# Optimization experiments

Hardware: AMD Instinct MI355X
Metric: run time of the kernel (lower is better)

## Reference

```python
import jax, jax.numpy as jnp
from jax import lax
import numpy as np

B, H, W, C = 4, 64, 64, 128
L = H * W
DI = 2 * C   # mamba d_inner (expand=2)
NS = 16      # d_state
R = C // 16  # dt_rank
K = 4        # d_conv
S = 4        # scan branches: fwd, bwd, extra1, extra2


def setup_inputs():
    key = jax.random.key(0)
    ks = jax.random.split(key, 20)
    g = lambda i, shape, s=0.02: jax.random.normal(ks[i], shape, jnp.float32) * s
    return {
        "I1": jax.random.normal(ks[0], (B, L, C), jnp.float32),
        "fusion_resi": jax.random.normal(ks[1], (B, L, C), jnp.float32),
        "I2": jax.random.normal(ks[2], (B, L, C), jnp.float32),
        "fusion": jax.random.normal(ks[3], (B, L, C), jnp.float32),
        "ln1_w": jnp.ones((C,)), "ln1_b": jnp.zeros((C,)),
        "ln2_w": jnp.ones((C,)), "ln2_b": jnp.zeros((C,)),
        "ln3_w": jnp.ones((C,)), "ln3_b": jnp.zeros((C,)),
        "sp_w": g(4, (1, 2, 5, 5), 0.1),
        "ca_w1": g(5, (C // 4, C), 0.05),
        "ca_w2": g(6, (C, C // 4), 0.05),
        "dw_w": g(7, (C, 1, 3, 3), 0.1),
        "dw_b": jnp.zeros((C,)),
        "in_proj_w": g(8, (2 * DI, C)),
        "in_proj1_w": g(9, (DI, C)),
        "in_proj2_w": g(10, (DI, C)),
        "conv_w": g(11, (S, DI, K), 0.1),
        "conv_b": jnp.zeros((S, DI)),
        "xproj_w": g(12, (S, R + 2 * NS, DI)),
        "dt_w": g(13, (S, DI, R), 0.1),
        "dt_b": jnp.full((S, DI), -4.6, jnp.float32),  # softplus -> dt ~ 0.01
        "A_log": jnp.broadcast_to(jnp.log(jnp.arange(1, NS + 1, dtype=jnp.float32)), (S, DI, NS)) * 1.0,
        "Dskip": jnp.ones((S, DI)),
        "out_w": g(14, (C, DI)),
        "test_h": H, "test_w": W,
    }


def ln(x, w, b):
    mu = x.mean(-1, keepdims=True)
    xc = x - mu
    v = (xc * xc).mean(-1, keepdims=True)
    return xc / jnp.sqrt(v + 1e-5) * w + b


def sp_att(x, w, h, wd):
    # x: (B, N, C) -> (B, N, 1) spatial attention map
    Bb = x.shape[0]
    m = jnp.concatenate([x.mean(2, keepdims=True), x.max(2, keepdims=True)], 2)
    m = m.transpose(0, 2, 1).reshape(Bb, 2, h, wd)
    o = lax.conv_general_dilated(m, w, (1, 1), [(2, 2), (2, 2)],
                                 dimension_numbers=("NCHW", "OIHW", "NCHW"))
    return jax.nn.sigmoid(o).reshape(Bb, 1, -1).transpose(0, 2, 1)


def mamba_m3(xf, e1, e2, in_proj_w, in_proj1_w, in_proj2_w, conv_w, conv_b,
             xproj_w, dt_w, dt_b, A_log, Dskip, out_w):
    Bb, Ll, _ = xf.shape
    xz = xf @ in_proj_w.T                       # (B,L,2DI)
    x, z = xz[..., :DI], xz[..., DI:]
    # 4 branches: forward, backward (flipped), extra_emb1, extra_emb2
    u = jnp.stack([x, x[:, ::-1], e1 @ in_proj1_w.T, e2 @ in_proj2_w.T], 0)  # (S,B,L,DI)

    def causal_dwconv(xb, w, b):                # xb (B,L,DI)
        xp = jnp.pad(xb.transpose(0, 2, 1), ((0, 0), (0, 0), (K - 1, 0)))
        o = lax.conv_general_dilated(xp, w[:, None, :], (1,), "VALID",
                                     feature_group_count=DI,
                                     dimension_numbers=("NCH", "OIH", "NCH"))
        return (o + b[None, :, None]).transpose(0, 2, 1)

    uc = jax.nn.silu(jax.vmap(causal_dwconv)(u, conv_w, conv_b))        # (S,B,L,DI)
    proj = jnp.einsum("sbld,spd->sblp", uc, xproj_w)
    dt = jax.nn.softplus(jnp.einsum("sblr,sdr->sbld", proj[..., :R], dt_w)
                         + dt_b[:, None, None, :])                      # (S,B,L,DI)
    Bm, Cm = proj[..., R:R + NS], proj[..., R + NS:]                    # (S,B,L,NS)
    A = -jnp.exp(A_log)                                                 # (S,DI,NS)

    def step(h, inp):
        dt_t, B_t, C_t, u_t = inp                                       # (S,B,DI),(S,B,NS),(S,B,NS),(S,B,DI)
        dA = jnp.exp(dt_t[..., None] * A[:, None])                      # (S,B,DI,NS)
        h = h * dA + (dt_t * u_t)[..., None] * B_t[:, :, None, :]
        return h, jnp.einsum("sbdn,sbn->sbd", h, C_t)

    xs = tuple(t.transpose(2, 0, 1, 3) for t in (dt, Bm, Cm, uc))
    h0 = jnp.zeros((S, Bb, DI, NS), xf.dtype)
    _, ys = lax.scan(step, h0, xs)                                      # (L,S,B,DI)
    y = ys.transpose(1, 2, 0, 3) + uc * Dskip[:, None, None, :]         # (S,B,L,DI)
    y_tot = y[0] + y[1][:, ::-1] + y[2] + y[3]
    return (y_tot * jax.nn.silu(z)) @ out_w.T


def reference(I1, fusion_resi, I2, fusion, ln1_w, ln1_b, ln2_w, ln2_b, ln3_w,
              ln3_b, sp_w, ca_w1, ca_w2, dw_w, dw_b, in_proj_w, in_proj1_w,
              in_proj2_w, conv_w, conv_b, xproj_w, dt_w, dt_b, A_log, Dskip,
              out_w, test_h, test_w):
    fusion_resi = fusion + fusion_resi
    fusion = ln(fusion_resi, ln1_w, ln1_b)
    I2 = ln(I2 * sp_att(I2, sp_w, test_h, test_w), ln2_w, ln2_b)
    I1 = ln(I1 * sp_att(I1, sp_w, test_h, test_w), ln3_w, ln3_b)
    # note: original applies norm1/norm2/norm3 a second time here (faithful)
    gf = mamba_m3(ln(fusion, ln1_w, ln1_b), ln(I2, ln2_w, ln2_b),
                  ln(I1, ln3_w, ln3_b), in_proj_w, in_proj1_w, in_proj2_w,
                  conv_w, conv_b, xproj_w, dt_w, dt_b, A_log, Dskip, out_w)
    Bb, _, Cc = gf.shape
    f4 = gf.transpose(0, 2, 1).reshape(Bb, Cc, test_h, test_w)
    # ChannelAttention1 (already returns x*sig) then extra *fusion per source
    fc = lambda v: jnp.maximum(v @ ca_w1.T, 0.0) @ ca_w2.T
    sig = jax.nn.sigmoid(fc(f4.mean((2, 3))) + fc(f4.max((2, 3))))[:, :, None, None]
    f4 = (f4 * sig) * f4
    dw = lax.conv_general_dilated(f4, dw_w, (1, 1), [(1, 1), (1, 1)],
                                  feature_group_count=Cc,
                                  dimension_numbers=("NCHW", "OIHW", "NCHW"))
    dw = dw + dw_b[None, :, None, None]
    out = (dw + f4).reshape(Bb, Cc, -1).transpose(0, 2, 1)
    return out, fusion_resi
```

## Files before the change

kernel.cpp:

```cpp
#include <hip/hip_runtime.h>

#define DEVI __device__ __forceinline__

static constexpr int BB=4, CC=128, LLn=4096, DI=256, NS=16, RR=8, SS=4;
static constexpr int PP = RR + 2*NS;
static constexpr int CT = 64, NCH = LLn/CT;
static constexpr size_t BLC  = (size_t)BB*LLn*CC;
static constexpr size_t BLD  = (size_t)BB*LLn*DI;
static constexpr size_t SBLD = (size_t)SS*BLD;
static constexpr size_t SBLP = (size_t)SS*BB*LLn*PP;

static constexpr int OW_LN1W=0, OW_LN1B=128, OW_LN2W=256, OW_LN2B=384, OW_LN3W=512, OW_LN3B=640,
 OW_SPW=768, OW_CAW1=820, OW_CAW2=4916, OW_DWW=9012, OW_DWB=10164, OW_IPW=10292,
 OW_IP1W=75828, OW_IP2W=108596, OW_CVW=141364, OW_CVB=145460, OW_XPW=146484,
 OW_DTW=187444, OW_DTB=195636, OW_ALOG=196660, OW_DSK=213044, OW_OUTW=214068;
static constexpr int NW_RAW = 246836;
static constexpr int NW_END = 246848;

__constant__ int c_woff[22] = {OW_LN1W,OW_LN1B,OW_LN2W,OW_LN2B,OW_LN3W,OW_LN3B,OW_SPW,OW_CAW1,
 OW_CAW2,OW_DWW,OW_DWB,OW_IPW,OW_IP1W,OW_IP2W,OW_CVW,OW_CVB,OW_XPW,OW_DTW,OW_DTB,OW_ALOG,
 OW_DSK,OW_OUTW};
__constant__ int c_wsz[22]  = {128,128,128,128,128,128,50,4096,4096,1152,128,65536,32768,32768,
 4096,1024,40960,8192,1024,16384,1024,32768};

static constexpr size_t O_XF   = NW_END;
static constexpr size_t O_E1   = O_XF + BLC;
static constexpr size_t O_E2   = O_E1 + BLC;
static constexpr size_t O_Z    = O_E2 + BLC;
static constexpr size_t O_U    = O_Z + BLD;
static constexpr size_t O_UC   = O_U + SBLD;
static constexpr size_t O_PROJ = O_UC + SBLD;
static constexpr size_t O_SDT  = O_PROJ + SBLP;
static constexpr size_t O_H    = O_SDT + (size_t)SS*BB*NCH*DI;
static constexpr size_t O_M    = O_H + (size_t)SS*BB*NCH*DI*NS;
static constexpr size_t O_S    = O_M + 2*(size_t)BB*2*LLn;
static constexpr size_t O_GF   = O_S + 2*(size_t)BB*LLn;
static constexpr size_t O_PART = O_GF + BLC;
static constexpr size_t O_SIG  = O_PART + 2*(size_t)BB*32*CC;
static constexpr size_t WS_END = O_SIG + (size_t)BB*CC;

typedef __attribute__((ext_vector_type(8))) short short8v;
typedef __attribute__((ext_vector_type(4))) float f32x4;

DEVI float bfu2f(unsigned short s){ union{unsigned u; float f;} c; c.u = ((unsigned)s)<<16; return c.f; }
DEVI unsigned short f2bfu(float f){ union{float f; unsigned u;} c; c.f=f;
  unsigned r = c.u + 0x7FFFu + ((c.u>>16)&1u); return (unsigned short)(r>>16); }
DEVI bool bfmode(const void* ln1w){ return *(const unsigned*)ln1w == 0x3F803F80u; }
DEVI float2 ldin2(const void* p, int i, bool isbf){
  if(isbf){ unsigned v = *(const unsigned*)((const unsigned short*)p + i);
    return make_float2(bfu2f((unsigned short)(v & 0xFFFFu)), bfu2f((unsigned short)(v >> 16))); }
  const float* f = (const float*)p + i; return make_float2(f[0], f[1]);
}
DEVI float wsum(float v){
#pragma unroll
  for(int o=32;o;o>>=1) v += __shfl_xor(v,o,64);
  return v; }
DEVI float wmaxr(float v){
#pragma unroll
  for(int o=32;o;o>>=1) v = fmaxf(v, __shfl_xor(v,o,64));
  return v; }
DEVI float sigf(float x){ return 1.f/(1.f+__expf(-x)); }
DEVI float2 ln_wave(float2 x, const float* Wf, int ow, int ob, int lane){
  float mu = wsum(x.x + x.y) * (1.f/(float)CC);
  float dx = x.x - mu, dy = x.y - mu;
  float var = wsum(dx*dx + dy*dy) * (1.f/(float)CC);
  float rs = rsqrtf(var + 1e-5f);
  int c = 2*lane;
  return make_float2(dx*rs*Wf[ow+c] + Wf[ob+c], dy*rs*Wf[ow+c+1] + Wf[ob+c+1]);
}

struct Srcs { const void* p[22]; };

__global__ void k_xwpad(unsigned* __restrict__ xw32){
  int i = blockIdx.x*256 + threadIdx.x;
  xw32[i] = 0u;
}

__global__ void k_wcvt(Srcs s, float* __restrict__ ws,
                       unsigned short* __restrict__ wip, unsigned short* __restrict__ wob,
                       unsigned short* __restrict__ xw){
  bool isbf = bfmode(s.p[0]);
  int idx = blockIdx.x*256 + threadIdx.x;
  if(idx >= NW_RAW) return;
  int t = 0;
  while(t < 21 && idx >= c_woff[t+1]) t++;
  int j = idx - c_woff[t];
  if(j >= c_wsz[t]) return;
  float v = isbf ? bfu2f(((const unsigned short*)s.p[t])[j]) : ((const float*)s.p[t])[j];
  ws[idx] = v;
  if(t==11)      wip[j]         = f2bfu(v);
  else if(t==12) wip[65536+j]   = f2bfu(v);
  else if(t==13) wip[98304+j]   = f2bfu(v);
  else if(t==21) wob[j]         = f2bfu(v);
  else if(t==16){
    int sid = j / 10240, rem = j % 10240;
    xw[((size_t)sid*64 + rem/256)*256 + (rem%256)] = f2bfu(v);
  }
}

__global__ void k_fuse(const void* fus, const void* fres, const void* ln1raw,
                       float* __restrict__ ws, float* __restrict__ outf,
                       unsigned short* __restrict__ xbf){
  bool isbf = bfmode(ln1raw);
  int lane = threadIdx.x & 63, wv = threadIdx.x >> 6;
  int row = blockIdx.x*4 + wv;
  int base = row*CC;
  float2 a = ldin2(fus, base+2*lane, isbf);
  float2 b = ldin2(fres, base+2*lane, isbf);
  float2 fr = make_float2(a.x+b.x, a.y+b.y);
  *(float2*)(outf + BLC + base + 2*lane) = fr;
  float2 y = ln_wave(fr, ws, OW_LN1W, OW_LN1B, lane);
  y = ln_wave(y, ws, OW_LN1W, OW_LN1B, lane);
  unsigned pk = (unsigned)f2bfu(y.x) | ((unsigned)f2bfu(y.y)<<16);
  *(unsigned*)&xbf[base + 2*lane] = pk;
}

__global__ void k_meanmax(const void* I1, const void* I2, const void* ln1raw, float* __restrict__ ws){
  bool isbf = bfmode(ln1raw);
  int lane = threadIdx.x & 63, wv = threadIdx.x >> 6;
  int g = blockIdx.x*4 + wv;
  int ten = g & 1, row = g >> 1;
  const void* src = ten ? I2 : I1;
  float2 x = ldin2(src, row*CC + 2*lane, isbf);
  float sm = wsum(x.x + x.y) * (1.f/(float)CC);
  float mx = wmaxr(fmaxf(x.x, x.y));
  if(lane == 0){
    int b = row >> 12, l = row & 4095;
    float* mt = ws + O_M + (size_t)ten*(BB*2*LLn);
    mt[(size_t)b*2*LLn + l] = sm;
    mt[(size_t)b*2*LLn + LLn + l] = mx;
  }
}

__global__ void k_spconv(float* __restrict__ ws){
  int idx = blockIdx.x*256 + threadIdx.x;
  int ten = idx >> 14, b = (idx>>12)&3, l = idx & 4095;
  int h = l >> 6, w = l & 63;
  const float* mt = ws + O_M + (size_t)ten*(BB*2*LLn) + (size_t)b*2*LLn;
  float acc = 0.f;
  for(int ci=0; ci<2; ci++)
    for(int kh=0; kh<5; kh++){
      int hh = h + kh - 2; if((unsigned)hh >= 64u) continue;
      for(int kw=0; kw<5; kw++){
        int wn = w + kw - 2; if((unsigned)wn >= 64u) continue;
        acc += mt[(size_t)ci*LLn + hh*64 + wn] * ws[OW_SPW + ci*25 + kh*5 + kw];
      }
    }
  ws[O_S + (size_t)ten*(BB*LLn) + (size_t)b*LLn + l] = sigf(acc);
}

__global__ void k_escale(const void* I1, const void* I2, const void* ln1raw,
                         float* __restrict__ ws, unsigned short* __restrict__ xbf){
  bool isbf = bfmode(ln1raw);
  int lane = threadIdx.x & 63, wv = threadIdx.x >> 6;
  int g = blockIdx.x*4 + wv;
  int ten = g & 1, row = g >> 1;
  const void* src = ten ? I1 : I2;
  float sc = ws[O_S + (ten ? 0 : (size_t)BB*LLn) + row];
  float2 x = ldin2(src, row*CC + 2*lane, isbf);
  x.x *= sc; x.y *= sc;
  int ow = ten ? OW_LN3W : OW_LN2W, ob = ten ? OW_LN3B : OW_LN2B;
  float2 y = ln_wave(x, ws, ow, ob, lane);
  y = ln_wave(y, ws, ow, ob, lane);
  unsigned short* eb = xbf + (ten ? 2*BLC : BLC);
  unsigned pk = (unsigned)f2bfu(y.x) | ((unsigned)f2bfu(y.y)<<16);
  *(unsigned*)&eb[row*CC + 2*lane] = pk;
}

__global__ __launch_bounds__(256) void k_gemm_bf(const unsigned short* __restrict__ Abf,
    const unsigned short* __restrict__ Wbf, float* __restrict__ out,
    int Kd, int N, int mode, float* __restrict__ u, float* __restrict__ z){
  __shared__ unsigned short As[64*64];
  __shared__ unsigned short Bs[64*64];
  const int tid = threadIdx.x, lane = tid & 63, w = tid >> 6;
  const int n0 = blockIdx.x*64, m0 = blockIdx.y*64;
  const int g = lane >> 4, rlo = lane & 15;
  if(mode == 2) Wbf += (size_t)(m0 >> 14) * (64*256);
  f32x4 acc[4];
#pragma unroll
  for(int i=0;i<4;i++) acc[i] = (f32x4){0.f,0.f,0.f,0.f};
  const int nk = Kd >> 6;
  for(int kt=0; kt<nk; kt++){
#pragma unroll
    for(int it=0; it<2; it++){
      int idx = it*256 + tid, r = idx>>3, c = idx&7;
      uint4 av = *(const uint4*)&Abf[(size_t)(m0+r)*Kd + kt*64 + c*8];
      uint4 bv = *(const uint4*)&Wbf[(size_t)(n0+r)*Kd + kt*64 + c*8];
      int sw = (c*16) ^ ((r&7)<<4);
      *(uint4*)((char*)As + r*128 + sw) = av;
      *(uint4*)((char*)Bs + r*128 + sw) = bv;
    }
    __syncthreads();
#pragma unroll
    for(int ks=0; ks<2; ks++){
      int kb = ks*64 + g*16;
      int brow = w*16 + rlo;
      short8v bf = *(short8v*)((char*)Bs + brow*128 + (kb ^ ((rlo&7)<<4)));
#pragma unroll
      for(int rt=0; rt<4; rt++){
        int arow = rt*16 + rlo;
        short8v af = *(short8v*)((char*)As + arow*128 + (kb ^ ((rlo&7)<<4)));
        acc[rt] = __builtin_amdgcn_mfma_f32_16x16x32_bf16(af, bf, acc[rt], 0, 0, 0);
      }
    }
    __syncthreads();
  }
#pragma unroll
  for(int rt=0; rt<4; rt++){
#pragma unroll
    for(int j=0; j<4; j++){
      int m = m0 + rt*16 + g*4 + j;
      int n = n0 + w*16 + rlo;
      float val = acc[rt][j];
      if(mode != 1){
        if(n < N) out[(size_t)m*N + n] = val;
      } else {
        int b = m >> 12, l = m & (LLn-1);
        if(n < DI){
          u[((size_t)b*LLn + l)*DI + n] = val;
        } else {
          z[((size_t)b*LLn + l)*DI + (n-DI)] = val;
        }
      }
    }
  }
}

__global__ void k_conv(float* __restrict__ ws, unsigned short* __restrict__ ucbf){
  int t = blockIdx.x*256 + threadIdx.x;
  int d4 = t & 63, l = (t>>6)&4095, sb = t>>18, s = sb>>2, b = sb&3;
  int d0 = d4*4;
  const float* wp = ws + OW_CVW + ((size_t)s*DI + d0)*4;
  float wv[16];
#pragma unroll
  for(int q=0;q<16;q++) wv[q] = wp[q];
  float4 acc = *(const float4*)&ws[OW_CVB + s*DI + d0];
  const bool rev = (s == 1);
  const float* ub = ws + O_U + (rev ? ((size_t)b*LLn)*DI : ((size_t)sb*LLn)*DI);
#pragma unroll
  for(int k=0;k<4;k++){
    int lk = l - 3 + k;
    if(lk >= 0){
      int li = rev ? (LLn-1-lk) : lk;
      float4 uv = *(const float4*)&ub[(size_t)li*DI + d0];
      acc.x += wv[0*4+k]*uv.x; acc.y += wv[1*4+k]*uv.y;
      acc.z += wv[2*4+k]*uv.z; acc.w += wv[3*4+k]*uv.w;
    }
  }
  acc.x *= sigf(acc.x); acc.y *= sigf(acc.y); acc.z *= sigf(acc.z); acc.w *= sigf(acc.w);
  ushort4 o4; o4.x=f2bfu(acc.x); o4.y=f2bfu(acc.y); o4.z=f2bfu(acc.z); o4.w=f2bfu(acc.w);
  *(ushort4*)&ucbf[((size_t)sb*LLn + l)*DI + d0] = o4;
}

template<bool PH3>
__global__ __launch_bounds__(256) void k_scan(float* __restrict__ ws,
                                              const unsigned short* __restrict__ ucbf){
  __shared__ float pl[CT*PP];
  int ch = blockIdx.x & (NCH-1), sb = blockIdx.x >> 6, s = sb >> 2;
  int d = threadIdx.x;
  size_t prow = ((size_t)sb*LLn + (size_t)ch*CT)*PP;
#pragma unroll
  for(int i=0;i<10;i++){ int idx = i*256 + threadIdx.x; pl[idx] = ws[O_PROJ + prow + idx]; }
  __syncthreads();
  float4 dtw0 = *(const float4*)&ws[OW_DTW + ((size_t)s*DI + d)*RR];
  float4 dtw1 = *(const float4*)&ws[OW_DTW + ((size_t)s*DI + d)*RR + 4];
  float dtb = ws[OW_DTB + s*DI + d];
  float an2[NS]; bool fast = true;
#pragma unroll
  for(int n=0;n<NS;n++){
    float a = -__expf(ws[OW_ALOG + ((size_t)s*DI + d)*NS + n]);
    an2[n] = a * 1.44269504f;
    fast = fast && (fabsf(a + (float)(n+1)) < 1e-4f);
  }
  float4 h0,h1,h2,h3;
  size_t hb = (((size_t)sb*NCH + ch)*DI + d)*NS;
  float* H = ws + O_H;
  if(PH3){
    h0 = *(const float4*)&H[hb];    h1 = *(const float4*)&H[hb+4];
    h2 = *(const float4*)&H[hb+8];  h3 = *(const float4*)&H[hb+12];
  } else {
    h0=h1=h2=h3=make_float4(0.f,0.f,0.f,0.f);
  }
  float dsk = PH3 ? ws[OW_DSK + s*DI + d] : 0.f;
  float sdt = 0.f;
  size_t ub = ((size_t)sb*LLn + (size_t)ch*CT)*DI + d;
  if(fast){
    for(int ll=0; ll<CT; ll++){
      const float* pr = &pl[ll*PP];
      float4 p0 = *(const float4*)pr, p1 = *(const float4*)(pr+4);
      float x = dtb + p0.x*dtw0.x + p0.y*dtw0.y + p0.z*dtw0.z + p0.w*dtw0.w
                    + p1.x*dtw1.x + p1.y*dtw1.y + p1.z*dtw1.z + p1.w*dtw1.w;
      float dt = (x > 15.f) ? x : __logf(1.f + __expf(x));
      float ut = bfu2f(ucbf[ub + (size_t)ll*DI]);
      float du = dt*ut;
      float e = __expf(-dt);
      float e2 = e*e, e4 = e2*e2;
      float4 da = make_float4(e, e2, e2*e, e4);
      float4 B0 = *(const float4*)(pr+8),  B1 = *(const float4*)(pr+12),
             B2 = *(const float4*)(pr+16), B3 = *(const float4*)(pr+20);
      if(PH3){
        float4 C0 = *(const float4*)(pr+24), C1 = *(const float4*)(pr+28),
               C2 = *(const float4*)(pr+32), C3 = *(const float4*)(pr+36);
        float y;
        h0.x = fmaf(h0.x, da.x, du*B0.x); y  = h0.x*C0.x;
        h0.y = fmaf(h0.y, da.y, du*B0.y); y = fmaf(h0.y, C0.y, y);
        h0.z = fmaf(h0.z, da.z, du*B0.z); y = fmaf(h0.z, C0.z, y);
        h0.w = fmaf(h0.w, da.w, du*B0.w); y = fmaf(h0.w, C0.w, y);
        da.x *= e4; da.y *= e4; da.z *= e4; da.w *= e4;
        h1.x = fmaf(h1.x, da.x, du*B1.x); y = fmaf(h1.x, C1.x, y);
        h1.y = fmaf(h1.y, da.y, du*B1.y); y = fmaf(h1.y, C1.y, y);
        h1.z = fmaf(h1.z, da.z, du*B1.z); y = fmaf(h1.z, C1.z, y);
        h1.w = fmaf(h1.w, da.w, du*B1.w); y = fmaf(h1.w, C1.w, y);
        da.x *= e4; da.y *= e4; da.z *= e4; da.w *= e4;
        h2.x = fmaf(h2.x, da.x, du*B2.x); y = fmaf(h2.x, C2.x, y);
        h2.y = fmaf(h2.y, da.y, du*B2.y); y = fmaf(h2.y, C2.y, y);
        h2.z = fmaf(h2.z, da.z, du*B2.z); y = fmaf(h2.z, C2.z, y);
        h2.w = fmaf(h2.w, da.w, du*B2.w); y = fmaf(h2.w, C2.w, y);
        da.x *= e4; da.y *= e4; da.z *= e4; da.w *= e4;
        h3.x = fmaf(h3.x, da.x, du*B3.x); y = fmaf(h3.x, C3.x, y);
        h3.y = fmaf(h3.y, da.y, du*B3.y); y = fmaf(h3.y, C3.y, y);
        h3.z = fmaf(h3.z, da.z, du*B3.z); y = fmaf(h3.z, C3.z, y);
        h3.w = fmaf(h3.w, da.w, du*B3.w); y = fmaf(h3.w, C3.w, y);
        ws[O_U + ub + (size_t)ll*DI] = y + ut*dsk;
      } else {
        h0.x = fmaf(h0.x, da.x, du*B0.x); h0.y = fmaf(h0.y, da.y, du*B0.y);
        h0.z = fmaf(h0.z, da.z, du*B0.z); h0.w = fmaf(h0.w, da.w, du*B0.w);
        da.x *= e4; da.y *= e4; da.z *= e4; da.w *= e4;
        h1.x = fmaf(h1.x, da.x, du*B1.x); h1.y = fmaf(h1.y, da.y, du*B1.y);
        h1.z = fmaf(h1.z, da.z, du*B1.z); h1.w = fmaf(h1.w, da.w, du*B1.w);
        da.x *= e4; da.y *= e4; da.z *= e4; da.w *= e4;
        h2.x = fmaf(h2.x, da.x, du*B2.x); h2.y = fmaf(h2.y, da.y, du*B2.y);
        h2.z = fmaf(h2.z, da.z, du*B2.z); h2.w = fmaf(h2.w, da.w, du*B2.w);
        da.x *= e4; da.y *= e4; da.z *= e4; da.w *= e4;
        h3.x = fmaf(h3.x, da.x, du*B3.x); h3.y = fmaf(h3.y, da.y, du*B3.y);
        h3.z = fmaf(h3.z, da.z, du*B3.z); h3.w = fmaf(h3.w, da.w, du*B3.w);
        sdt += dt;
      }
    }
  } else {
    float h[NS];
    h[0]=h0.x;h[1]=h0.y;h[2]=h0.z;h[3]=h0.w; h[4]=h1.x;h[5]=h1.y;h[6]=h1.z;h[7]=h1.w;
    h[8]=h2.x;h[9]=h2.y;h[10]=h2.z;h[11]=h2.w; h[12]=h3.x;h[13]=h3.y;h[14]=h3.z;h[15]=h3.w;
    for(int ll=0; ll<CT; ll++){
      const float* pr = &pl[ll*PP];
      float x = dtb;
      x += pr[0]*dtw0.x + pr[1]*dtw0.y + pr[2]*dtw0.z + pr[3]*dtw0.w;
      x += pr[4]*dtw1.x + pr[5]*dtw1.y + pr[6]*dtw1.z + pr[7]*dtw1.w;
      float dt = (x > 15.f) ? x : __logf(1.f + __expf(x));
      float ut = bfu2f(ucbf[ub + (size_t)ll*DI]);
      float du = dt*ut;
      if(PH3){
        float y = 0.f;
#pragma unroll
        for(int n=0;n<NS;n++){ float da = exp2f(an2[n]*dt); h[n] = h[n]*da + du*pr[RR+n]; y += h[n]*pr[RR+NS+n]; }
        ws[O_U + ub + (size_t)ll*DI] = y + ut*dsk;
      } else {
#pragma unroll
        for(int n=0;n<NS;n++){ float da = exp2f(an2[n]*dt); h[n] = h[n]*da + du*pr[RR+n]; }
        sdt += dt;
      }
    }
    h0=make_float4(h[0],h[1],h[2],h[3]); h1=make_float4(h[4],h[5],h[6],h[7]);
    h2=make_float4(h[8],h[9],h[10],h[11]); h3=make_float4(h[12],h[13],h[14],h[15]);
  }
  if(!PH3){
    *(float4*)&H[hb]    = h0; *(float4*)&H[hb+4]  = h1;
    *(float4*)&H[hb+8]  = h2; *(float4*)&H[hb+12] = h3;
    ws[O_SDT + ((size_t)sb*NCH + ch)*DI + d] = sdt;
  }
}

__global__ void k_scan2(float* __restrict__ ws){
  int t = blockIdx.x*256 + threadIdx.x;
  int n = t & (NS-1), d = (t>>4) & (DI-1), sb = t >> 12, s = sb >> 2;
  float an2 = -__expf(ws[OW_ALOG + ((size_t)s*DI + d)*NS + n]) * 1.44269504f;
  float hin = 0.f;
  float* H = ws + O_H;
  for(int c=0;c<NCH;c++){
    size_t hi = (((size_t)sb*NCH + c)*DI + d)*NS + n;
    float he = H[hi];
    float sd = ws[O_SDT + ((size_t)sb*NCH + c)*DI + d];
    H[hi] = hin;
    hin = he + exp2f(an2*sd)*hin;
  }
}

__global__ void k_gate(float* __restrict__ ws, unsigned short* __restrict__ gbf){
  int t = blockIdx.x*256 + threadIdx.x;
  int d4 = t & 63, l = (t>>6)&4095, b = t>>18;
  int d0 = d4*4;
  const float* y = ws + O_U;
  size_t i0 = ((size_t)(0*BB+b)*LLn + l)*DI + d0;
  size_t i1 = ((size_t)(1*BB+b)*LLn + (LLn-1-l))*DI + d0;
  size_t i2 = ((size_t)(2*BB+b)*LLn + l)*DI + d0;
  size_t i3 = ((size_t)(3*BB+b)*LLn + l)*DI + d0;
  float4 a = *(const float4*)&y[i0], bb4 = *(const float4*)&y[i1];
  float4 c = *(const float4*)&y[i2], dd = *(const float4*)&y[i3];
  size_t zi = ((size_t)b*LLn + l)*DI + d0;
  float4 zv = *(const float4*)&ws[O_Z + zi];
  float4 g;
  g.x = (a.x+bb4.x+c.x+dd.x) * (zv.x*sigf(zv.x));
  g.y = (a.y+bb4.y+c.y+dd.y) * (zv.y*sigf(zv.y));
  g.z = (a.z+bb4.z+c.z+dd.z) * (zv.z*sigf(zv.z));
  g.w = (a.w+bb4.w+c.w+dd.w) * (zv.w*sigf(zv.w));
  uint2 pk;
  pk.x = (unsigned)f2bfu(g.x) | ((unsigned)f2bfu(g.y)<<16);
  pk.y = (unsigned)f2bfu(g.z) | ((unsigned)f2bfu(g.w)<<16);
  *(uint2*)&gbf[zi] = pk;
}

__global__ void k_redmm(float* __restrict__ ws){
  int b = blockIdx.x >> 5, seg = blockIdx.x & 31, c = threadIdx.x;
  const float* gf = ws + O_GF;
  float sm = 0.f, mx = -3e38f;
  size_t base = ((size_t)b*LLn + (size_t)seg*128)*CC + c;
  for(int i=0;i<128;i++){ float v = gf[base + (size_t)i*CC]; sm += v; mx = fmaxf(mx, v); }
  ws[O_PART + ((size_t)b*32 + seg)*CC + c] = sm;
  ws[O_PART + (size_t)BB*32*CC + ((size_t)b*32 + seg)*CC + c] = mx;
}

__global__ void k_catt(float* __restrict__ ws){
  __shared__ float vm[CC], vx[CC], hm[32], hx[32];
  int b = blockIdx.x, c = threadIdx.x;
  float sm = 0.f, mx = -3e38f;
  for(int seg=0;seg<32;seg++){
    sm += ws[O_PART + ((size_t)b*32+seg)*CC + c];
    mx = fmaxf(mx, ws[O_PART + (size_t)BB*32*CC + ((size_t)b*32+seg)*CC + c]);
  }
  vm[c] = sm * (1.f/(float)LLn); vx[c] = mx;
  __syncthreads();
  if(c < 32){
    float am = 0.f, ax = 0.f;
    for(int k=0;k<CC;k++){ float w1 = ws[OW_CAW1 + c*CC + k]; am += vm[k]*w1; ax += vx[k]*w1; }
    hm[c] = fmaxf(am, 0.f); hx[c] = fmaxf(ax, 0.f);
  }
  __syncthreads();
  float om = 0.f, ox = 0.f;
  for(int k=0;k<32;k++){ float w2 = ws[OW_CAW2 + c*32 + k]; om += hm[k]*w2; ox += hx[k]*w2; }
  ws[O_SIG + (size_t)b*CC + c] = sigf(om + ox);
}

__global__ void k_final(float* __restrict__ ws, float* __restrict__ outf){
  int t = blockIdx.x*256 + threadIdx.x;
  int c4 = t & 31, l = (t>>5)&4095, b = t>>17;
  int h = l>>6, w = l&63;
  const float* gf = ws + O_GF;
  float4 sg = *(const float4*)&ws[O_SIG + (size_t)b*CC + c4*4];
  size_t rb = ((size_t)b*LLn)*CC;
  float4 gc = *(const float4*)&gf[rb + (size_t)l*CC + c4*4];
  float4 fc = make_float4(gc.x*gc.x*sg.x, gc.y*gc.y*sg.y, gc.z*gc.z*sg.z, gc.w*gc.w*sg.w);
  float4 acc = *(const float4*)&ws[OW_DWB + c4*4];
  float wv[4][9];
#pragma unroll
  for(int j=0;j<4;j++)
#pragma unroll
    for(int q=0;q<9;q++) wv[j][q] = ws[OW_DWW + (c4*4+j)*9 + q];
#pragma unroll
  for(int kh=0;kh<3;kh++){
    int hh = h + kh - 1; if((unsigned)hh >= 64u) continue;
#pragma unroll
    for(int kw=0;kw<3;kw++){
      int wn = w + kw - 1; if((unsigned)wn >= 64u) continue;
      float4 g = *(const float4*)&gf[rb + (size_t)(hh*64+wn)*CC + c4*4];
      int q = kh*3+kw;
      acc.x += wv[0][q]*g.x*g.x*sg.x;
      acc.y += wv[1][q]*g.y*g.y*sg.y;
      acc.z += wv[2][q]*g.z*g.z*sg.z;
      acc.w += wv[3][q]*g.w*g.w*sg.w;
    }
  }
  float4 o = make_float4(acc.x+fc.x, acc.y+fc.y, acc.z+fc.z, acc.w+fc.w);
  size_t ob = ((size_t)b*LLn + l)*CC + c4*4;
  *(float4*)&outf[ob] = o;
}

extern "C" void kernel_launch(void* const* d_in, const int* in_sizes, int n_in,
                              void* d_out, int out_size, void* d_ws, size_t ws_size,
                              hipStream_t stream){
  (void)in_sizes; (void)n_in; (void)out_size;
  if(ws_size < WS_END*sizeof(float)) return;
  float* ws = (float*)d_ws;
  float* outf = (float*)d_out;
  const void* I1 = d_in[0]; const void* FRES = d_in[1];
  const void* I2 = d_in[2]; const void* FUS  = d_in[3];
  const void* LN1RAW = d_in[4];

  unsigned short* xbf   = (unsigned short*)(ws + O_H);
  unsigned short* gbf   = xbf;
  unsigned short* wipbf = (unsigned short*)(ws + O_GF);
  unsigned short* wobf  = (unsigned short*)(ws + O_PART);
  unsigned short* xwbf  = (unsigned short*)(ws + O_XF);
  unsigned short* ucbf  = (unsigned short*)(ws + O_UC);

  Srcs sr;
  for(int i=0;i<22;i++) sr.p[i] = d_in[4+i];
  k_xwpad<<<128, 256, 0, stream>>>((unsigned*)xwbf);
  k_wcvt<<<(NW_RAW+255)/256, 256, 0, stream>>>(sr, ws, wipbf, wobf, xwbf);
  k_fuse<<<4096, 256, 0, stream>>>(FUS, FRES, LN1RAW, ws, outf, xbf);
  k_meanmax<<<8192, 256, 0, stream>>>(I1, I2, LN1RAW, ws);
  k_spconv<<<128, 256, 0, stream>>>(ws);
  k_escale<<<8192, 256, 0, stream>>>(I1, I2, LN1RAW, ws, xbf);
  k_gemm_bf<<<dim3(8,256), 256, 0, stream>>>(xbf,         wipbf,       nullptr,        128, 512, 1, ws+O_U, ws+O_Z);
  k_gemm_bf<<<dim3(4,256), 256, 0, stream>>>(xbf+BLC,     wipbf+65536, ws+O_U+2*BLD,   128, 256, 0, nullptr, nullptr);
  k_gemm_bf<<<dim3(4,256), 256, 0, stream>>>(xbf+2*BLC,   wipbf+98304, ws+O_U+3*BLD,   128, 256, 0, nullptr, nullptr);
  k_conv<<<16384, 256, 0, stream>>>(ws, ucbf);
  k_gemm_bf<<<dim3(1,1024), 256, 0, stream>>>(ucbf, xwbf, ws+O_PROJ, 256, 40, 2, nullptr, nullptr);
  k_scan<false><<<SS*BB*NCH, 256, 0, stream>>>(ws, ucbf);
  k_scan2<<<256, 256, 0, stream>>>(ws);
  k_scan<true><<<SS*BB*NCH, 256, 0, stream>>>(ws, ucbf);
  k_gate<<<4096, 256, 0, stream>>>(ws, gbf);
  k_gemm_bf<<<dim3(2,256), 256, 0, stream>>>(gbf, wobf, ws+O_GF, 256, 128, 0, nullptr, nullptr);
  k_redmm<<<128, 128, 0, stream>>>(ws);
  k_catt<<<4, 128, 0, stream>>>(ws);
  k_final<<<2048, 256, 0, stream>>>(ws, outf);
}
```

Baseline: 285.0 us.

## Store in-proj outputs and scan outputs as bf16 and register-block the conv

The in_proj GEMMs now write the u branches as bf16 instead of fp32, and the scan writes its y outputs into the same buffer as bf16. The depthwise causal conv reads bf16 input and computes four consecutive positions per thread, reusing a sliding window of loaded rows, and the gate kernel reads bf16 y. This is meant to halve the memory traffic on these large intermediates and cut redundant conv loads. It costs extra rounding of u and y to bf16, which may reduce accuracy.

```diff
diff --git a/kernel.cpp b/kernel.cpp
--- a/kernel.cpp
+++ b/kernel.cpp
@@ -45,6 +45,8 @@
 DEVI float bfu2f(unsigned short s){ union{unsigned u; float f;} c; c.u = ((unsigned)s)<<16; return c.f; }
 DEVI unsigned short f2bfu(float f){ union{float f; unsigned u;} c; c.f=f;
   unsigned r = c.u + 0x7FFFu + ((c.u>>16)&1u); return (unsigned short)(r>>16); }
+DEVI float4 bf4(uint2 v){ return make_float4(bfu2f((unsigned short)(v.x&0xFFFFu)), bfu2f((unsigned short)(v.x>>16)),
+                                             bfu2f((unsigned short)(v.y&0xFFFFu)), bfu2f((unsigned short)(v.y>>16))); }
 DEVI bool bfmode(const void* ln1w){ return *(const unsigned*)ln1w == 0x3F803F80u; }
 DEVI float2 ldin2(const void* p, int i, bool isbf){
   if(isbf){ unsigned v = *(const unsigned*)((const unsigned short*)p + i);
@@ -169,7 +171,7 @@
 
 __global__ __launch_bounds__(256) void k_gemm_bf(const unsigned short* __restrict__ Abf,
     const unsigned short* __restrict__ Wbf, float* __restrict__ out,
-    int Kd, int N, int mode, float* __restrict__ u, float* __restrict__ z){
+    int Kd, int N, int mode, unsigned short* __restrict__ ub16, float* __restrict__ z){
   __shared__ unsigned short As[64*64];
   __shared__ unsigned short Bs[64*64];
   const int tid = threadIdx.x, lane = tid & 63, w = tid >> 6;
@@ -212,44 +214,52 @@
       int m = m0 + rt*16 + g*4 + j;
       int n = n0 + w*16 + rlo;
       float val = acc[rt][j];
-      if(mode != 1){
+      if(mode == 1){
+        int b = m >> 12, l = m & (LLn-1);
+        if(n < DI) ub16[((size_t)b*LLn + l)*DI + n] = f2bfu(val);
+        else       z[((size_t)b*LLn + l)*DI + (n-DI)] = val;
+      } else if(mode == 3){
+        ub16[(size_t)m*N + n] = f2bfu(val);
+      } else {
         if(n < N) out[(size_t)m*N + n] = val;
-      } else {
-        int b = m >> 12, l = m & (LLn-1);
-        if(n < DI){
-          u[((size_t)b*LLn + l)*DI + n] = val;
-        } else {
-          z[((size_t)b*LLn + l)*DI + (n-DI)] = val;
-        }
       }
     }
   }
 }
 
-__global__ void k_conv(float* __restrict__ ws, unsigned short* __restrict__ ucbf){
+__global__ void k_conv(const float* __restrict__ ws, const unsigned short* __restrict__ ubf,
+                       unsigned short* __restrict__ ucbf){
   int t = blockIdx.x*256 + threadIdx.x;
-  int d4 = t & 63, l = (t>>6)&4095, sb = t>>18, s = sb>>2, b = sb&3;
-  int d0 = d4*4;
+  int dg = t & 63, lg = (t>>6) & 1023, sb = t >> 16, s = sb >> 2, b = sb & 3;
+  int d0 = dg*4, l0 = lg*4;
+  float wv[16];
   const float* wp = ws + OW_CVW + ((size_t)s*DI + d0)*4;
-  float wv[16];
 #pragma unroll
   for(int q=0;q<16;q++) wv[q] = wp[q];
-  float4 acc = *(const float4*)&ws[OW_CVB + s*DI + d0];
+  float4 cb = *(const float4*)&ws[OW_CVB + s*DI + d0];
   const bool rev = (s == 1);
-  const float* ub = ws + O_U + (rev ? ((size_t)b*LLn)*DI : ((size_t)sb*LLn)*DI);
-#pragma unroll
-  for(int k=0;k<4;k++){
-    int lk = l - 3 + k;
-    if(lk >= 0){
-      int li = rev ? (LLn-1-lk) : lk;
-      float4 uv = *(const float4*)&ub[(size_t)li*DI + d0];
-      acc.x += wv[0*4+k]*uv.x; acc.y += wv[1*4+k]*uv.y;
-      acc.z += wv[2*4+k]*uv.z; acc.w += wv[3*4+k]*uv.w;
-    }
-  }
-  acc.x *= sigf(acc.x); acc.y *= sigf(acc.y); acc.z *= sigf(acc.z); acc.w *= sigf(acc.w);
-  ushort4 o4; o4.x=f2bfu(acc.x); o4.y=f2bfu(acc.y); o4.z=f2bfu(acc.z); o4.w=f2bfu(acc.w);
-  *(ushort4*)&ucbf[((size_t)sb*LLn + l)*DI + d0] = o4;
+  const unsigned short* ub = ubf + (rev ? (size_t)b*LLn : (size_t)sb*LLn)*DI;
+  float4 w0, w1, w2;
+  {
+    int lm;
+    lm = l0-3; w0 = (lm<0)?make_float4(0,0,0,0):bf4(*(const uint2*)&ub[(size_t)(rev?(LLn-1-lm):lm)*DI + d0]);
+    lm = l0-2; w1 = (lm<0)?make_float4(0,0,0,0):bf4(*(const uint2*)&ub[(size_t)(rev?(LLn-1-lm):lm)*DI + d0]);
+    lm = l0-1; w2 = (lm<0)?make_float4(0,0,0,0):bf4(*(const uint2*)&ub[(size_t)(rev?(LLn-1-lm):lm)*DI + d0]);
+  }
+#pragma unroll
+  for(int r=0;r<4;r++){
+    int l = l0 + r;
+    float4 w3 = bf4(*(const uint2*)&ub[(size_t)(rev?(LLn-1-l):l)*DI + d0]);
+    float4 acc;
+    acc.x = cb.x + wv[0]*w0.x + wv[1]*w1.x + wv[2]*w2.x + wv[3]*w3.x;
+    acc.y = cb.y + wv[4]*w0.y + wv[5]*w1.y + wv[6]*w2.y + wv[7]*w3.y;
+    acc.z = cb.z + wv[8]*w0.z + wv[9]*w1.z + wv[10]*w2.z + wv[11]*w3.z;
+    acc.w = cb.w + wv[12]*w0.w + wv[13]*w1.w + wv[14]*w2.w + wv[15]*w3.w;
+    acc.x *= sigf(acc.x); acc.y *= sigf(acc.y); acc.z *= sigf(acc.z); acc.w *= sigf(acc.w);
+    ushort4 o4; o4.x=f2bfu(acc.x); o4.y=f2bfu(acc.y); o4.z=f2bfu(acc.z); o4.w=f2bfu(acc.w);
+    *(ushort4*)&ucbf[((size_t)sb*LLn + l)*DI + d0] = o4;
+    w0 = w1; w1 = w2; w2 = w3;
+  }
 }
 
 template<bool PH3>
@@ -262,6 +272,7 @@
 #pragma unroll
   for(int i=0;i<10;i++){ int idx = i*256 + threadIdx.x; pl[idx] = ws[O_PROJ + prow + idx]; }
   __syncthreads();
+  unsigned short* ybf = (unsigned short*)(ws + O_U);
   float4 dtw0 = *(const float4*)&ws[OW_DTW + ((size_t)s*DI + d)*RR];
   float4 dtw1 = *(const float4*)&ws[OW_DTW + ((size_t)s*DI + d)*RR + 4];
   float dtb = ws[OW_DTB + s*DI + d];
@@ -321,7 +332,7 @@
         h3.y = fmaf(h3.y, da.y, du*B3.y); y = fmaf(h3.y, C3.y, y);
         h3.z = fmaf(h3.z, da.z, du*B3.z); y = fmaf(h3.z, C3.z, y);
         h3.w = fmaf(h3.w, da.w, du*B3.w); y = fmaf(h3.w, C3.w, y);
-        ws[O_U + ub + (size_t)ll*DI] = y + ut*dsk;
+        ybf[ub + (size_t)ll*DI] = f2bfu(y + ut*dsk);
       } else {
         h0.x = fmaf(h0.x, da.x, du*B0.x); h0.y = fmaf(h0.y, da.y, du*B0.y);
         h0.z = fmaf(h0.z, da.z, du*B0.z); h0.w = fmaf(h0.w, da.w, du*B0.w);
@@ -353,7 +364,7 @@
         float y = 0.f;
 #pragma unroll
         for(int n=0;n<NS;n++){ float da = exp2f(an2[n]*dt); h[n] = h[n]*da + du*pr[RR+n]; y += h[n]*pr[RR+NS+n]; }
-        ws[O_U + ub + (size_t)ll*DI] = y + ut*dsk;
+        ybf[ub + (size_t)ll*DI] = f2bfu(y + ut*dsk);
       } else {
 #pragma unroll
         for(int n=0;n<NS;n++){ float da = exp2f(an2[n]*dt); h[n] = h[n]*da + du*pr[RR+n]; }
@@ -389,13 +400,15 @@
   int t = blockIdx.x*256 + threadIdx.x;
   int d4 = t & 63, l = (t>>6)&4095, b = t>>18;
   int d0 = d4*4;
-  const float* y = ws + O_U;
+  const unsigned short* ybf = (const unsigned short*)(ws + O_U);
   size_t i0 = ((size_t)(0*BB+b)*LLn + l)*DI + d0;
   size_t i1 = ((size_t)(1*BB+b)*LLn + (LLn-1-l))*DI + d0;
   size_t i2 = ((size_t)(2*BB+b)*LLn + l)*DI + d0;
   size_t i3 = ((size_t)(3*BB+b)*LLn + l)*DI + d0;
-  float4 a = *(const float4*)&y[i0], bb4 = *(const float4*)&y[i1];
-  float4 c = *(const float4*)&y[i2], dd = *(const float4*)&y[i3];
+  float4 a = bf4(*(const uint2*)&ybf[i0]);
+  float4 bb4 = bf4(*(const uint2*)&ybf[i1]);
+  float4 c = bf4(*(const uint2*)&ybf[i2]);
+  float4 dd = bf4(*(const uint2*)&ybf[i3]);
   size_t zi = ((size_t)b*LLn + l)*DI + d0;
   float4 zv = *(const float4*)&ws[O_Z + zi];
   float4 g;
@@ -491,6 +504,7 @@
   unsigned short* wobf  = (unsigned short*)(ws + O_PART);
   unsigned short* xwbf  = (unsigned short*)(ws + O_XF);
   unsigned short* ucbf  = (unsigned short*)(ws + O_UC);
+  unsigned short* ubf   = (unsigned short*)(ws + O_U);
 
   Srcs sr;
   for(int i=0;i<22;i++) sr.p[i] = d_in[4+i];
@@ -500,10 +514,10 @@
   k_meanmax<<<8192, 256, 0, stream>>>(I1, I2, LN1RAW, ws);
   k_spconv<<<128, 256, 0, stream>>>(ws);
   k_escale<<<8192, 256, 0, stream>>>(I1, I2, LN1RAW, ws, xbf);
-  k_gemm_bf<<<dim3(8,256), 256, 0, stream>>>(xbf,         wipbf,       nullptr,        128, 512, 1, ws+O_U, ws+O_Z);
-  k_gemm_bf<<<dim3(4,256), 256, 0, stream>>>(xbf+BLC,     wipbf+65536, ws+O_U+2*BLD,   128, 256, 0, nullptr, nullptr);
-  k_gemm_bf<<<dim3(4,256), 256, 0, stream>>>(xbf+2*BLC,   wipbf+98304, ws+O_U+3*BLD,   128, 256, 0, nullptr, nullptr);
-  k_conv<<<16384, 256, 0, stream>>>(ws, ucbf);
+  k_gemm_bf<<<dim3(8,256), 256, 0, stream>>>(xbf,         wipbf,       nullptr,      128, 512, 1, ubf,        ws+O_Z);
+  k_gemm_bf<<<dim3(4,256), 256, 0, stream>>>(xbf+BLC,     wipbf+65536, nullptr,      128, 256, 3, ubf+2*BLD,  nullptr);
+  k_gemm_bf<<<dim3(4,256), 256, 0, stream>>>(xbf+2*BLC,   wipbf+98304, nullptr,      128, 256, 3, ubf+3*BLD,  nullptr);
+  k_conv<<<4096, 256, 0, stream>>>(ws, ubf, ucbf);
   k_gemm_bf<<<dim3(1,1024), 256, 0, stream>>>(ucbf, xwbf, ws+O_PROJ, 256, 40, 2, nullptr, nullptr);
   k_scan<false><<<SS*BB*NCH, 256, 0, stream>>>(ws, ucbf);
   k_scan2<<<256, 256, 0, stream>>>(ws);
```

After: 241.0 us. -15.4%, faster.
